# Performance work log

Measured on AMD Instinct MI355X. Metric: run time of the kernel, lower is better.

The kernel has to match this reference:

```python
import jax, jax.numpy as jnp
import numpy as np

OUT, IN = 11008, 4096  # weight matrix shape (out_features, in_features)
TOKENS = 64


def setup_inputs() -> dict:
    key = jax.random.key(0)
    k1, k2, k3 = jax.random.split(key, 3)
    x = jax.random.normal(k1, (TOKENS, IN), dtype=jnp.float32)
    # packed 1-bit weights: each int holds 8 sign bits (values 0..255)
    bp = jax.random.randint(k2, (OUT * IN // 8,), 0, 256, dtype=jnp.int32)
    # per-output-row scale, broadcasts over bit_mat rows
    scale = jax.random.uniform(k3, (OUT, 1), dtype=jnp.float32) * 0.02 + 0.001
    return {"x": x, "bp": bp, "scale": scale}


def _unpack_bits(bp):
    # bp: [N] ints in [0,256). Extract bits MSB-first (i=0 -> bit 7), map {0,1}->{-1,+1}.
    shifts = jnp.arange(7, -1, -1, dtype=jnp.int32)  # [8]
    bits = (bp[:, None] >> shifts) & 1               # [N, 8]
    return (bits.reshape(-1) * 2 - 1)                # [N*8] in {-1, +1}


def reference(x, bp, scale):
    bit_mat = _unpack_bits(bp).reshape(OUT, IN).astype(x.dtype)  # [OUT, IN]
    w = bit_mat * scale                                          # [OUT, IN]
    return x @ w.T                                               # [TOKENS, OUT]
```

## Files before the change

kernel.cpp:

```cpp
#include <hip/hip_runtime.h>
#include <stdint.h>

using short8 = __attribute__((ext_vector_type(8))) short;
using f32x4  = __attribute__((ext_vector_type(4))) float;

#define OUT_F 11008
#define IN_F  4096
#define TOK   64
#define WPR   (IN_F/8)
#define BN    128
#define KSPLIT 8
#define KQ    (IN_F/KSPLIT)
#define BK    256
#define NCH   (KQ/BK)
#define NBLK  (OUT_F/BN)
#define PARTF (TOK*OUT_F)

__device__ __forceinline__ unsigned short f2bf(float f) {
    uint32_t u = __float_as_uint(f);
    u += 0x7FFFu + ((u >> 16) & 1u);
    return (unsigned short)(u >> 16);
}

__device__ __forceinline__ short8 unpack_w(uint32_t w) {
    union { short8 v; uint32_t u[4]; } r;
#pragma unroll
    for (int p = 0; p < 4; ++p) {
        uint32_t lo = (w << (8  + 2*p)) & 0x8000u;
        uint32_t hi = (w << (25 + 2*p)) & 0x80000000u;
        r.u[p] = 0xBF80BF80u ^ lo ^ hi;
    }
    return r.v;
}

__global__ __launch_bounds__(256) void gemm_kernel(const float* __restrict__ x,
                                                   const uint32_t* __restrict__ bp,
                                                   const float* __restrict__ scale,
                                                   float* __restrict__ pw) {
    __shared__ __align__(128) unsigned char xs[TOK * BK * 2];

    const int bid  = blockIdx.x;
    const int nblk = bid % NBLK;
    const int q    = bid / NBLK;
    const int n0   = nblk * BN;
    const int tid  = threadIdx.x;
    const int wv   = tid >> 6;
    const int lane = tid & 63;
    const int l15  = lane & 15;
    const int lg   = lane >> 4;

    const uint32_t* b0p = bp + (size_t)(n0 + wv*32 + l15) * WPR + q*(KQ/8) + lg;
    const uint32_t* b1p = b0p + 16 * WPR;
    uint32_t wA[NCH][8], wB[NCH][8];
#pragma unroll
    for (int c = 0; c < NCH; ++c)
#pragma unroll
        for (int kk = 0; kk < 8; ++kk) {
            wA[c][kk] = b0p[c*32 + kk*4];
            wB[c][kk] = b1p[c*32 + kk*4];
        }
    const float sc0 = scale[n0 + wv*32 + l15];
    const float sc1 = scale[n0 + wv*32 + 16 + l15];

    f32x4 acc[2][4];
#pragma unroll
    for (int nf = 0; nf < 2; ++nf)
#pragma unroll
        for (int mt = 0; mt < 4; ++mt) acc[nf][mt] = (f32x4){0.f, 0.f, 0.f, 0.f};

    for (int c = 0; c < NCH; ++c) {
        if (c) __syncthreads();
        const float* xc = x + q*KQ + c*BK;
#pragma unroll
        for (int it = 0; it < 16; ++it) {
            int f  = tid + it*256;
            int r  = f >> 6;
            int c4 = f & 63;
            float4 v = *(const float4*)(xc + (size_t)r*IN_F + c4*4);
            uint32_t lo = (uint32_t)f2bf(v.x) | ((uint32_t)f2bf(v.y) << 16);
            uint32_t hi = (uint32_t)f2bf(v.z) | ((uint32_t)f2bf(v.w) << 16);
            int a = (r*512 + c4*8) ^ ((r & 7) << 4);
            *(uint2*)(xs + a) = make_uint2(lo, hi);
        }
        __syncthreads();

#pragma unroll
        for (int kk = 0; kk < 8; ++kk) {
            short8 b0 = unpack_w(wA[c][kk]);
            short8 b1 = unpack_w(wB[c][kk]);
#pragma unroll
            for (int mt = 0; mt < 4; ++mt) {
                int row = mt*16 + l15;
                int ba  = (row*512 + kk*64 + lg*16) ^ ((row & 7) << 4);
                short8 af = *(const short8*)(xs + ba);
                acc[0][mt] = __builtin_amdgcn_mfma_f32_16x16x32_bf16(af, b0, acc[0][mt], 0, 0, 0);
                acc[1][mt] = __builtin_amdgcn_mfma_f32_16x16x32_bf16(af, b1, acc[1][mt], 0, 0, 0);
            }
        }
    }

    float* base = pw + (size_t)q * PARTF;
#pragma unroll
    for (int mt = 0; mt < 4; ++mt)
#pragma unroll
        for (int j = 0; j < 4; ++j) {
            int m = mt*16 + lg*4 + j;
            base[(size_t)m*OUT_F + n0 + wv*32 + l15]      = acc[0][mt][j]*sc0;
            base[(size_t)m*OUT_F + n0 + wv*32 + 16 + l15] = acc[1][mt][j]*sc1;
        }
}

__global__ __launch_bounds__(256) void reduce_kernel(const float4* __restrict__ pw,
                                                     float4* __restrict__ out) {
    int i = blockIdx.x * 256 + threadIdx.x;
    float4 s = pw[i];
#pragma unroll
    for (int qq = 1; qq < KSPLIT; ++qq) {
        float4 t = pw[(size_t)qq*(PARTF/4) + i];
        s.x += t.x; s.y += t.y; s.z += t.z; s.w += t.w;
    }
    out[i] = s;
}

extern "C" void kernel_launch(void* const* d_in, const int* in_sizes, int n_in,
                              void* d_out, int out_size, void* d_ws, size_t ws_size,
                              hipStream_t stream) {
    const float*    x     = (const float*)d_in[0];
    const uint32_t* bp    = (const uint32_t*)d_in[1];
    const float*    scale = (const float*)d_in[2];
    float* pw = (float*)d_ws;

    gemm_kernel<<<dim3(NBLK*KSPLIT), dim3(256), 0, stream>>>(x, bp, scale, pw);
    reduce_kernel<<<dim3((PARTF/4)/256), dim3(256), 0, stream>>>((const float4*)pw,
                                                                 (float4*)d_out);
}
```

Measured before the change: 100.9 us.

## Store split-K partials as bf16 and halve the K-split factor

Partial sums from the split-K GEMM are now rounded to bf16 before being written to the workspace, and the reduce kernel reads eight bf16 values per thread and accumulates them in fp32. KSPLIT drops from 8 to 4, which doubles the per-block K range and the weight registers held per thread, and the chunk loop is fully unrolled. The aim is to cut the partial-sum write and read traffic, roughly a quarter of the previous volume. The cost is fewer blocks for parallelism, more register pressure, and extra rounding error in the partial sums.

```diff
diff --git a/kernel.cpp b/kernel.cpp
--- a/kernel.cpp
+++ b/kernel.cpp
@@ -9,7 +9,7 @@
 #define TOK   64
 #define WPR   (IN_F/8)
 #define BN    128
-#define KSPLIT 8
+#define KSPLIT 4
 #define KQ    (IN_F/KSPLIT)
 #define BK    256
 #define NCH   (KQ/BK)
@@ -36,7 +36,7 @@
 __global__ __launch_bounds__(256) void gemm_kernel(const float* __restrict__ x,
                                                    const uint32_t* __restrict__ bp,
                                                    const float* __restrict__ scale,
-                                                   float* __restrict__ pw) {
+                                                   unsigned short* __restrict__ pw) {
     __shared__ __align__(128) unsigned char xs[TOK * BK * 2];
 
     const int bid  = blockIdx.x;
@@ -68,14 +68,14 @@
 #pragma unroll
         for (int mt = 0; mt < 4; ++mt) acc[nf][mt] = (f32x4){0.f, 0.f, 0.f, 0.f};
 
+#pragma unroll
     for (int c = 0; c < NCH; ++c) {
         if (c) __syncthreads();
         const float* xc = x + q*KQ + c*BK;
 #pragma unroll
         for (int it = 0; it < 16; ++it) {
-            int f  = tid + it*256;
-            int r  = f >> 6;
-            int c4 = f & 63;
+            int r  = wv + it*4;
+            int c4 = lane;
             float4 v = *(const float4*)(xc + (size_t)r*IN_F + c4*4);
             uint32_t lo = (uint32_t)f2bf(v.x) | ((uint32_t)f2bf(v.y) << 16);
             uint32_t hi = (uint32_t)f2bf(v.z) | ((uint32_t)f2bf(v.w) << 16);
@@ -99,27 +99,34 @@
         }
     }
 
-    float* base = pw + (size_t)q * PARTF;
+    unsigned short* base = pw + (size_t)q * PARTF;
 #pragma unroll
     for (int mt = 0; mt < 4; ++mt)
 #pragma unroll
         for (int j = 0; j < 4; ++j) {
             int m = mt*16 + lg*4 + j;
-            base[(size_t)m*OUT_F + n0 + wv*32 + l15]      = acc[0][mt][j]*sc0;
-            base[(size_t)m*OUT_F + n0 + wv*32 + 16 + l15] = acc[1][mt][j]*sc1;
+            base[(size_t)m*OUT_F + n0 + wv*32 + l15]      = f2bf(acc[0][mt][j]*sc0);
+            base[(size_t)m*OUT_F + n0 + wv*32 + 16 + l15] = f2bf(acc[1][mt][j]*sc1);
         }
 }
 
-__global__ __launch_bounds__(256) void reduce_kernel(const float4* __restrict__ pw,
-                                                     float4* __restrict__ out) {
+__global__ __launch_bounds__(256) void reduce_kernel(const unsigned short* __restrict__ pw,
+                                                     float* __restrict__ out) {
     int i = blockIdx.x * 256 + threadIdx.x;
-    float4 s = pw[i];
+    float s[8];
 #pragma unroll
-    for (int qq = 1; qq < KSPLIT; ++qq) {
-        float4 t = pw[(size_t)qq*(PARTF/4) + i];
-        s.x += t.x; s.y += t.y; s.z += t.z; s.w += t.w;
+    for (int e = 0; e < 8; ++e) s[e] = 0.f;
+#pragma unroll
+    for (int qq = 0; qq < KSPLIT; ++qq) {
+        short8 v = ((const short8*)(pw + (size_t)qq*PARTF))[i];
+#pragma unroll
+        for (int e = 0; e < 8; ++e)
+            s[e] += __uint_as_float(((uint32_t)(unsigned short)v[e]) << 16);
     }
-    out[i] = s;
+    float4 o0 = {s[0], s[1], s[2], s[3]};
+    float4 o1 = {s[4], s[5], s[6], s[7]};
+    ((float4*)out)[2*i]   = o0;
+    ((float4*)out)[2*i+1] = o1;
 }
 
 extern "C" void kernel_launch(void* const* d_in, const int* in_sizes, int n_in,
@@ -128,9 +135,8 @@
     const float*    x     = (const float*)d_in[0];
     const uint32_t* bp    = (const uint32_t*)d_in[1];
     const float*    scale = (const float*)d_in[2];
-    float* pw = (float*)d_ws;
+    unsigned short* pw = (unsigned short*)d_ws;
 
     gemm_kernel<<<dim3(NBLK*KSPLIT), dim3(256), 0, stream>>>(x, bp, scale, pw);
-    reduce_kernel<<<dim3((PARTF/4)/256), dim3(256), 0, stream>>>((const float4*)pw,
-                                                                 (float4*)d_out);
+    reduce_kernel<<<dim3((PARTF/8)/256), dim3(256), 0, stream>>>(pw, (float*)d_out);
 }
```

After: 98.04 us. -2.8%, faster.
